# Kernel tuning notes

Hardware: AMD Instinct MI355X
Metric: run time of the kernel (lower is better)

Reference implementation:

```python
import jax, jax.numpy as jnp
import numpy as np

D_MODEL = 1024
NUM_HEADS = 16
HEAD_DIM = D_MODEL // NUM_HEADS
THETA = 10000.0
B, S = 1, 2048


def setup_inputs() -> dict:
    key = jax.random.key(0)
    ks = jax.random.split(key, 7)
    sc = 0.02
    return {
        "query": jax.random.normal(ks[0], (B, S, D_MODEL), jnp.float32),
        "key": jax.random.normal(ks[1], (B, S, D_MODEL), jnp.float32),
        "value": jax.random.normal(ks[2], (B, S, D_MODEL), jnp.float32),
        "qkv_w": jax.random.normal(ks[3], (3 * D_MODEL, D_MODEL), jnp.float32) * sc,
        "qkv_b": jax.random.normal(ks[4], (3 * D_MODEL,), jnp.float32) * sc,
        "out_w": jax.random.normal(ks[5], (D_MODEL, D_MODEL), jnp.float32) * sc,
        "out_b": jax.random.normal(ks[6], (D_MODEL,), jnp.float32) * sc,
    }


def _rope_cos_sin(seq_len, head_dim, dtype):
    # freqs_for='lang': inv_freq = theta^(-2i/d), i = 0..d/2-1
    inv_freq = 1.0 / (THETA ** (jnp.arange(0, head_dim, 2, dtype=jnp.float32) / head_dim))
    t = jnp.arange(seq_len, dtype=jnp.float32)
    freqs = jnp.outer(t, inv_freq)                      # [S, d/2]
    emb = jnp.concatenate([freqs, freqs], axis=-1)      # [S, d] (non-interleaved)
    return jnp.cos(emb).astype(dtype), jnp.sin(emb).astype(dtype)


def _rotate_half(x):
    half = x.shape[-1] // 2
    return jnp.concatenate([-x[..., half:], x[..., :half]], axis=-1)


def reference(query, key, value, qkv_w, qkv_b, out_w, out_b):
    # NOTE: module computes q,k,v all from `query` (key/value args unused).
    b, s, d = query.shape
    qkv = query @ qkv_w.T + qkv_b                       # [B,S,3D]
    qkv = qkv.reshape(b, s, 3, NUM_HEADS, HEAD_DIM)
    qkv = jnp.transpose(qkv, (2, 0, 3, 1, 4))           # [3,B,H,S,hd]
    q, k, v = qkv[0], qkv[1], qkv[2]

    cos, sin = _rope_cos_sin(s, HEAD_DIM, query.dtype)  # [S,hd]
    q = q * cos + _rotate_half(q) * sin
    k = k * cos + _rotate_half(k) * sin

    scale = 1.0 / np.sqrt(HEAD_DIM)
    scores = jnp.einsum('bhqd,bhkd->bhqk', q, k) * scale
    attn = jax.nn.softmax(scores, axis=-1)
    ctx = jnp.einsum('bhqk,bhkd->bhqd', attn, v)        # [B,H,S,hd]
    ctx = jnp.transpose(ctx, (0, 2, 1, 3)).reshape(b, s, d)
    return ctx @ out_w.T + out_b
```

## Files before the change

kernel.cpp:

```cpp
#include <hip/hip_runtime.h>
#include <math.h>
#include <stdint.h>

#define SEQ 2048
#define DM  1024
#define NH  16
#define HD  64
#define TRI 3072
#define NSPLIT 4

typedef _Float16 half8 __attribute__((ext_vector_type(8)));
typedef _Float16 half4 __attribute__((ext_vector_type(4)));
typedef __fp16 fp16x2 __attribute__((ext_vector_type(2)));
typedef float f32x4 __attribute__((ext_vector_type(4)));

#define GLOAD_LDS16(g, l)                                       \
  __builtin_amdgcn_global_load_lds(                             \
      (__attribute__((address_space(1))) void*)(g),             \
      (__attribute__((address_space(3))) void*)(l), 16, 0, 0)

#define QSCALE 0.18033688011112042f

__global__ __launch_bounds__(256)
void cvt3(const float* __restrict__ s1, const float* __restrict__ s2,
          const float* __restrict__ s3, _Float16* __restrict__ d1,
          _Float16* __restrict__ d2, _Float16* __restrict__ d3,
          float2* __restrict__ tab, int n1, int n2) {
  int b = blockIdx.x;
  if (b >= 6144) {
    int i = (b - 6144) * 256 + threadIdx.x;
    int s = i >> 5, d = i & 31;
    float inv = exp2f((float)d * -0.4152410118609203f);
    float ang = (float)s * inv;
    float sn, cs;
    sincosf(ang, &sn, &cs);
    tab[i] = make_float2(cs, sn);
    return;
  }
  int i = (b * 256 + threadIdx.x) * 4;
  const float* s; _Float16* d;
  if (i < n1)            { s = s1; d = d1; }
  else if (i < n1 + n2)  { s = s2; d = d2; i -= n1; }
  else                   { s = s3; d = d3; i -= n1 + n2; }
  float4 v = *(const float4*)(s + i);
  union { _Float16 h[4]; uint2 u; } pk;
  pk.h[0] = (_Float16)v.x; pk.h[1] = (_Float16)v.y;
  pk.h[2] = (_Float16)v.z; pk.h[3] = (_Float16)v.w;
  *(uint2*)(d + i) = pk.u;
}

__global__ __launch_bounds__(256)
void gemm_qkv(const _Float16* __restrict__ A, const _Float16* __restrict__ B,
              const float* __restrict__ bias, const float2* __restrict__ tab,
              _Float16* __restrict__ Qo, _Float16* __restrict__ Ko,
              _Float16* __restrict__ Vo) {
  constexpr int K = DM;
  __shared__ _Float16 As[2][64 * 32];
  __shared__ _Float16 Bs[2][128 * 32];

  const int t = threadIdx.x, lane = t & 63, wv = t >> 6;
  const int l15 = lane & 15, l4 = lane >> 4;
  const int wr = wv >> 1, wc = wv & 1;
  const int bm = blockIdx.y * 64, bn = blockIdx.x * 128;

  auto stage = [&](int buf, int k0) {
    {
      int c = t;
      GLOAD_LDS16(A + (size_t)(bm + (c >> 2)) * K + k0 + (c & 3) * 8,
                  (char*)&As[buf][wv * 512]);
    }
    #pragma unroll
    for (int i = 0; i < 2; ++i) {
      int c = t + i * 256;
      GLOAD_LDS16(B + (size_t)(bn + (c >> 2)) * K + k0 + (c & 3) * 8,
                  (char*)&Bs[buf][(i * 256 + wv * 64) * 8]);
    }
  };

  f32x4 acc[2][4] = {};
  stage(0, 0);
  __syncthreads();

  const int nk = K / 32;
  for (int s = 0; s < nk; ++s) {
    int cur = s & 1;
    if (s + 1 < nk) stage(cur ^ 1, (s + 1) * 32);
    half8 af[2], bf[4];
    #pragma unroll
    for (int mf = 0; mf < 2; ++mf)
      af[mf] = *(const half8*)&As[cur][(wr * 32 + mf * 16 + l15) * 32 + l4 * 8];
    #pragma unroll
    for (int nf = 0; nf < 4; ++nf)
      bf[nf] = *(const half8*)&Bs[cur][(wc * 64 + nf * 16 + l15) * 32 + l4 * 8];
    __builtin_amdgcn_s_setprio(1);
    #pragma unroll
    for (int mf = 0; mf < 2; ++mf)
      #pragma unroll
      for (int nf = 0; nf < 4; ++nf)
        acc[mf][nf] = __builtin_amdgcn_mfma_f32_16x16x32_f16(
            af[mf], bf[nf], acc[mf][nf], 0, 0, 0);
    __builtin_amdgcn_s_setprio(0);
    __syncthreads();
  }

  const int sec = bn >> 10;
  float bv[4];
  #pragma unroll
  for (int nf = 0; nf < 4; ++nf) bv[nf] = bias[bn + wc * 64 + nf * 16 + l15];

  if (sec == 0) {
    #pragma unroll
    for (int mf = 0; mf < 2; ++mf)
      #pragma unroll
      for (int r = 0; r < 4; ++r) {
        int row = bm + wr * 32 + mf * 16 + l4 * 4 + r;
        float v0 = acc[mf][0][r] + bv[0];
        float v1 = acc[mf][1][r] + bv[1];
        float v2 = acc[mf][2][r] + bv[2];
        float v3 = acc[mf][3][r] + bv[3];
        float2 cs0 = tab[row * 32 + l15];
        float2 cs1 = tab[row * 32 + 16 + l15];
        float a0 = (v0 * cs0.x - v2 * cs0.y) * QSCALE;
        float a2 = (v2 * cs0.x + v0 * cs0.y) * QSCALE;
        float a1 = (v1 * cs1.x - v3 * cs1.y) * QSCALE;
        float a3 = (v3 * cs1.x + v1 * cs1.y) * QSCALE;
        _Float16* cr = Qo + (size_t)row * DM + bn + wc * 64 + l15;
        cr[0]  = (_Float16)a0; cr[16] = (_Float16)a1;
        cr[32] = (_Float16)a2; cr[48] = (_Float16)a3;
      }
  } else if (sec == 1) {
    const int hh = ((bn - 1024) >> 6) + wc;
    const int e = l15 & 7, hi = l15 >> 3;
    #pragma unroll
    for (int mf = 0; mf < 2; ++mf)
      #pragma unroll
      for (int r = 0; r < 4; ++r) {
        int row = bm + wr * 32 + mf * 16 + l4 * 4 + r;
        float v0 = acc[mf][0][r] + bv[0];
        float v1 = acc[mf][1][r] + bv[1];
        float v2 = acc[mf][2][r] + bv[2];
        float v3 = acc[mf][3][r] + bv[3];
        float2 cs0 = tab[row * 32 + l15];
        float2 cs1 = tab[row * 32 + 16 + l15];
        float a0 = v0 * cs0.x - v2 * cs0.y;
        float a2 = v2 * cs0.x + v0 * cs0.y;
        float a1 = v1 * cs1.x - v3 * cs1.y;
        float a3 = v3 * cs1.x + v1 * cs1.y;
        int kk = row & 63, kseg = row >> 6;
        int hkk = (kk & 3) | ((kk >> 1) & 4);
        size_t base = ((size_t)(hh * 32 + kseg) * 64 + kk) * 64;
        Ko[base + (((0 + hi) ^ hkk) * 8) + e] = (_Float16)a0;
        Ko[base + (((2 + hi) ^ hkk) * 8) + e] = (_Float16)a1;
        Ko[base + (((4 + hi) ^ hkk) * 8) + e] = (_Float16)a2;
        Ko[base + (((6 + hi) ^ hkk) * 8) + e] = (_Float16)a3;
      }
  } else {
    const int hh = ((bn - 2048) >> 6) + wc;
    #pragma unroll
    for (int mf = 0; mf < 2; ++mf) {
      int row0 = bm + wr * 32 + mf * 16 + l4 * 4;
      int kk0 = row0 & 63, kseg = row0 >> 6;
      #pragma unroll
      for (int nf = 0; nf < 4; ++nf) {
        int d = nf * 16 + l15;
        union { _Float16 hh4[4]; uint2 u; } pk;
        #pragma unroll
        for (int r = 0; r < 4; ++r)
          pk.hh4[r] = (_Float16)(acc[mf][nf][r] + bv[nf]);
        size_t off = ((size_t)(hh * 32 + kseg) * 64 + d) * 64 +
                     (((kk0 >> 3) ^ (d & 7)) * 8) + (kk0 & 7);
        *(uint2*)(Vo + off) = pk.u;
      }
    }
  }
}

__global__ __launch_bounds__(256)
void gemm_out(const _Float16* __restrict__ A, const _Float16* __restrict__ B,
              const float* __restrict__ bias, float* __restrict__ C) {
  constexpr int K = DM, N = DM;
  __shared__ _Float16 As[2][64 * 32];
  __shared__ _Float16 Bs[2][128 * 32];

  const int t = threadIdx.x, lane = t & 63, wv = t >> 6;
  const int l15 = lane & 15, l4 = lane >> 4;
  const int wr = wv >> 1, wc = wv & 1;
  const int bm = blockIdx.y * 64, bn = blockIdx.x * 128;

  auto stage = [&](int buf, int k0) {
    {
      int c = t;
      GLOAD_LDS16(A + (size_t)(bm + (c >> 2)) * K + k0 + (c & 3) * 8,
                  (char*)&As[buf][wv * 512]);
    }
    #pragma unroll
    for (int i = 0; i < 2; ++i) {
      int c = t + i * 256;
      GLOAD_LDS16(B + (size_t)(bn + (c >> 2)) * K + k0 + (c & 3) * 8,
                  (char*)&Bs[buf][(i * 256 + wv * 64) * 8]);
    }
  };

  f32x4 acc[2][4] = {};
  stage(0, 0);
  __syncthreads();

  const int nk = K / 32;
  for (int s = 0; s < nk; ++s) {
    int cur = s & 1;
    if (s + 1 < nk) stage(cur ^ 1, (s + 1) * 32);
    half8 af[2], bf[4];
    #pragma unroll
    for (int mf = 0; mf < 2; ++mf)
      af[mf] = *(const half8*)&As[cur][(wr * 32 + mf * 16 + l15) * 32 + l4 * 8];
    #pragma unroll
    for (int nf = 0; nf < 4; ++nf)
      bf[nf] = *(const half8*)&Bs[cur][(wc * 64 + nf * 16 + l15) * 32 + l4 * 8];
    __builtin_amdgcn_s_setprio(1);
    #pragma unroll
    for (int mf = 0; mf < 2; ++mf)
      #pragma unroll
      for (int nf = 0; nf < 4; ++nf)
        acc[mf][nf] = __builtin_amdgcn_mfma_f32_16x16x32_f16(
            af[mf], bf[nf], acc[mf][nf], 0, 0, 0);
    __builtin_amdgcn_s_setprio(0);
    __syncthreads();
  }

  float bv[4];
  #pragma unroll
  for (int nf = 0; nf < 4; ++nf) bv[nf] = bias[bn + wc * 64 + nf * 16 + l15];
  #pragma unroll
  for (int mf = 0; mf < 2; ++mf)
    #pragma unroll
    for (int r = 0; r < 4; ++r) {
      int row = bm + wr * 32 + mf * 16 + l4 * 4 + r;
      float* cr = C + (size_t)row * N + bn + wc * 64 + l15;
      cr[0]  = acc[mf][0][r] + bv[0];
      cr[16] = acc[mf][1][r] + bv[1];
      cr[32] = acc[mf][2][r] + bv[2];
      cr[48] = acc[mf][3][r] + bv[3];
    }
}

__global__ __launch_bounds__(256)
void attn_f16(const _Float16* __restrict__ Qg, const _Float16* __restrict__ Kg,
              const _Float16* __restrict__ Vg, _Float16* __restrict__ poA,
              _Float16* __restrict__ po3, float* __restrict__ pl) {
  __shared__ _Float16 Kl[2][64 * 64];
  __shared__ _Float16 Vt[2][64 * 64];

  const int t = threadIdx.x, lane = t & 63, wv = t >> 6;
  const int l15 = lane & 15, l4 = lane >> 4;
  const int bid = blockIdx.x;
  const int c = bid & 63, qb = bid >> 6;
  const int h = c & 15, z = c >> 4;
  const int q0 = qb * 64;
  const int seg0 = z * (SEQ / NSPLIT / 64);

  const _Float16* Qp = Qg + h * HD;
  const _Float16* Kbase = Kg + (size_t)h * 32 * 4096;
  const _Float16* Vbase = Vg + (size_t)h * 32 * 4096;

  half8 qf[2];
  {
    const _Float16* qrow = Qp + (size_t)(q0 + wv * 16 + l15) * DM;
    qf[0] = *(const half8*)(qrow + l4 * 8);
    qf[1] = *(const half8*)(qrow + 32 + l4 * 8);
  }

  auto issueKV = [&](int buf, int seg) {
    const _Float16* ks = Kbase + (size_t)seg * 4096;
    const _Float16* vs = Vbase + (size_t)seg * 4096;
    GLOAD_LDS16(ks + (size_t)t * 8,         (char*)&Kl[buf][(wv * 64) * 8]);
    GLOAD_LDS16(ks + (size_t)(t + 256) * 8, (char*)&Kl[buf][(256 + wv * 64) * 8]);
    GLOAD_LDS16(vs + (size_t)t * 8,         (char*)&Vt[buf][(wv * 64) * 8]);
    GLOAD_LDS16(vs + (size_t)(t + 256) * 8, (char*)&Vt[buf][(256 + wv * 64) * 8]);
  };

  f32x4 lacc = {0.f, 0.f, 0.f, 0.f};
  f32x4 o[4] = {};

  const int hk = (l15 & 3) | (((l15 >> 2) & 1) << 2);
  const int krow = 8 * (l15 >> 2) + (l15 & 3);

  issueKV(0, seg0);

  const int NT = SEQ / NSPLIT / 64;
  #pragma unroll 2
  for (int tt = 0; tt < NT; ++tt) {
    const int cur = tt & 1;
    asm volatile("s_waitcnt vmcnt(0)" ::: "memory");
    __builtin_amdgcn_s_barrier();
    __builtin_amdgcn_sched_barrier(0);
    if (tt + 1 < NT) issueKV(cur ^ 1, seg0 + tt + 1);

    f32x4 sT[4] = {};
    __builtin_amdgcn_s_setprio(1);
    #pragma unroll
    for (int ds = 0; ds < 2; ++ds)
      #pragma unroll
      for (int m = 0; m < 4; ++m) {
        int kappa = 32 * (m >> 1) + 4 * (m & 1) + krow;
        int cb = ds * 4 + l4;
        half8 kf = *(const half8*)((char*)Kl[cur] + kappa * 128 +
                                   ((cb ^ hk) * 16));
        sT[m] = __builtin_amdgcn_mfma_f32_16x16x32_f16(kf, qf[ds], sT[m], 0, 0, 0);
      }
    __builtin_amdgcn_s_setprio(0);

    half8 pB[2];
    #pragma unroll
    for (int s2 = 0; s2 < 2; ++s2) {
      union { fp16x2 h2[4]; half8 v; } pu;
      #pragma unroll
      for (int mh = 0; mh < 2; ++mh) {
        int m = s2 * 2 + mh;
        f32x4 p;
        #pragma unroll
        for (int r = 0; r < 4; ++r) p[r] = exp2f(sT[m][r]);
        lacc += p;
        pu.h2[mh * 2 + 0] = __builtin_amdgcn_cvt_pkrtz(p[0], p[1]);
        pu.h2[mh * 2 + 1] = __builtin_amdgcn_cvt_pkrtz(p[2], p[3]);
      }
      pB[s2] = pu.v;
    }

    __builtin_amdgcn_s_setprio(1);
    #pragma unroll
    for (int s2 = 0; s2 < 2; ++s2)
      #pragma unroll
      for (int nf = 0; nf < 4; ++nf) {
        half8 va = *(const half8*)((char*)Vt[cur] + (nf * 16 + l15) * 128 +
                                   (((s2 * 4 + l4) ^ (l15 & 7)) * 16));
        o[nf] = __builtin_amdgcn_mfma_f32_16x16x32_f16(va, pB[s2], o[nf], 0, 0, 0);
      }
    __builtin_amdgcn_s_setprio(0);
  }

  float lv = (lacc[0] + lacc[1]) + (lacc[2] + lacc[3]);
  lv += __shfl_xor(lv, 16);
  lv += __shfl_xor(lv, 32);
  _Float16* pz = (z < 3) ? (poA + (size_t)z * SEQ * DM) : po3;
  {
    int row = q0 + wv * 16 + l15;
    _Float16* pr = pz + (size_t)row * DM + h * HD + l4 * 4;
    #pragma unroll
    for (int nf = 0; nf < 4; ++nf) {
      union { fp16x2 h2[2]; uint2 u; } ou;
      ou.h2[0] = __builtin_amdgcn_cvt_pkrtz(o[nf][0], o[nf][1]);
      ou.h2[1] = __builtin_amdgcn_cvt_pkrtz(o[nf][2], o[nf][3]);
      *(uint2*)(pr + nf * 16) = ou.u;
    }
  }
  if (l4 == 0) {
    int q = q0 + wv * 16 + l15;
    pl[(z * NH + h) * SEQ + q] = lv;
  }
}

__global__ __launch_bounds__(256)
void merge4(const _Float16* __restrict__ poA, const _Float16* __restrict__ po3,
            const float* __restrict__ pl, _Float16* __restrict__ ctx) {
  int e = (blockIdx.x * 256 + threadIdx.x) * 8;
  int s = e >> 10, h = (e & 1023) >> 6;
  int idx = h * SEQ + s;
  float L = pl[idx] + pl[NH * SEQ + idx] + pl[2 * NH * SEQ + idx] +
            pl[3 * NH * SEQ + idx];
  float inv = 1.0f / L;
  half8 a = *(const half8*)(poA + e);
  half8 b = *(const half8*)(poA + (size_t)SEQ * DM + e);
  half8 cc = *(const half8*)(poA + 2 * (size_t)SEQ * DM + e);
  half8 d = *(const half8*)(po3 + e);
  half8 o;
  #pragma unroll
  for (int j = 0; j < 8; ++j)
    o[j] = (_Float16)((((float)a[j] + (float)b[j]) +
                       ((float)cc[j] + (float)d[j])) * inv);
  *(half8*)(ctx + e) = o;
}

extern "C" void kernel_launch(void* const* d_in, const int* in_sizes, int n_in,
                              void* d_out, int out_size, void* d_ws, size_t ws_size,
                              hipStream_t stream) {
  const float* query = (const float*)d_in[0];
  const float* qkv_w = (const float*)d_in[3];
  const float* qkv_b = (const float*)d_in[4];
  const float* out_w = (const float*)d_in[5];
  const float* out_b = (const float*)d_in[6];
  float* out = (float*)d_out;

  char* ws = (char*)d_ws;
  _Float16* Aq   = (_Float16*)ws;
  _Float16* Wqkv = (_Float16*)(ws + (4u << 20));
  _Float16* Qb   = (_Float16*)(ws + (12u << 20));
  _Float16* Kb   = (_Float16*)(ws + (16u << 20));
  _Float16* Vb   = (_Float16*)(ws + (20u << 20));
  _Float16* ctx  = (_Float16*)(ws + (24u << 20));
  float2*   tab  = (float2*)(ws + (28u << 20));
  _Float16* Wout = (_Float16*)(ws + (28u << 20) + (512u << 10));
  float*    pl   = (float*)(ws + (30u << 20) + (512u << 10));
  _Float16* poA  = (_Float16*)ws;
  _Float16* po3  = ctx;

  cvt3<<<6400, 256, 0, stream>>>(query, qkv_w, out_w, Aq, Wqkv, Wout, tab,
                                 SEQ * DM, TRI * DM);

  gemm_qkv<<<dim3(TRI / 128, SEQ / 64), 256, 0, stream>>>(
      Aq, Wqkv, qkv_b, tab, Qb, Kb, Vb);

  attn_f16<<<(SEQ / 64) * NH * NSPLIT, 256, 0, stream>>>(
      Qb, Kb, Vb, poA, po3, pl);

  merge4<<<SEQ * DM / 8 / 256, 256, 0, stream>>>(poA, po3, pl, ctx);

  gemm_out<<<dim3(DM / 128, SEQ / 64), 256, 0, stream>>>(ctx, Wout, out_b, out);
}
```

Before: 96.90 us.

## Fuse split-merge into output GEMM, enlarge QKV tiles, widen attention blocks

```diff
diff --git a/kernel.cpp b/kernel.cpp
--- a/kernel.cpp
+++ b/kernel.cpp
@@ -10,7 +10,6 @@
 #define NSPLIT 4
 
 typedef _Float16 half8 __attribute__((ext_vector_type(8)));
-typedef _Float16 half4 __attribute__((ext_vector_type(4)));
 typedef __fp16 fp16x2 __attribute__((ext_vector_type(2)));
 typedef float f32x4 __attribute__((ext_vector_type(4)));
 
@@ -55,19 +54,20 @@
               _Float16* __restrict__ Qo, _Float16* __restrict__ Ko,
               _Float16* __restrict__ Vo) {
   constexpr int K = DM;
-  __shared__ _Float16 As[2][64 * 32];
-  __shared__ _Float16 Bs[2][128 * 32];
+  __shared__ _Float16 As[3][128 * 32];
+  __shared__ _Float16 Bs[3][128 * 32];
 
   const int t = threadIdx.x, lane = t & 63, wv = t >> 6;
   const int l15 = lane & 15, l4 = lane >> 4;
   const int wr = wv >> 1, wc = wv & 1;
-  const int bm = blockIdx.y * 64, bn = blockIdx.x * 128;
+  const int bm = blockIdx.y * 128, bn = blockIdx.x * 128;
 
   auto stage = [&](int buf, int k0) {
-    {
-      int c = t;
+    #pragma unroll
+    for (int i = 0; i < 2; ++i) {
+      int c = t + i * 256;
       GLOAD_LDS16(A + (size_t)(bm + (c >> 2)) * K + k0 + (c & 3) * 8,
-                  (char*)&As[buf][wv * 512]);
+                  (char*)&As[buf][(i * 256 + wv * 64) * 8]);
     }
     #pragma unroll
     for (int i = 0; i < 2; ++i) {
@@ -77,30 +77,34 @@
     }
   };
 
-  f32x4 acc[2][4] = {};
+  f32x4 acc[4][4] = {};
   stage(0, 0);
-  __syncthreads();
+  stage(1, 32);
 
   const int nk = K / 32;
   for (int s = 0; s < nk; ++s) {
-    int cur = s & 1;
-    if (s + 1 < nk) stage(cur ^ 1, (s + 1) * 32);
-    half8 af[2], bf[4];
-    #pragma unroll
-    for (int mf = 0; mf < 2; ++mf)
-      af[mf] = *(const half8*)&As[cur][(wr * 32 + mf * 16 + l15) * 32 + l4 * 8];
+    int cur = s % 3;
+    if (s + 1 < nk) asm volatile("s_waitcnt vmcnt(4)" ::: "memory");
+    else            asm volatile("s_waitcnt vmcnt(0)" ::: "memory");
+    __builtin_amdgcn_s_barrier();
+    __builtin_amdgcn_sched_barrier(0);
+    if (s + 2 < nk) stage((s + 2) % 3, (s + 2) * 32);
+
+    half8 af[4], bf[4];
+    #pragma unroll
+    for (int mf = 0; mf < 4; ++mf)
+      af[mf] = *(const half8*)&As[cur][(wr * 64 + mf * 16 + l15) * 32 + l4 * 8];
     #pragma unroll
     for (int nf = 0; nf < 4; ++nf)
       bf[nf] = *(const half8*)&Bs[cur][(wc * 64 + nf * 16 + l15) * 32 + l4 * 8];
     __builtin_amdgcn_s_setprio(1);
     #pragma unroll
-    for (int mf = 0; mf < 2; ++mf)
+    for (int mf = 0; mf < 4; ++mf)
       #pragma unroll
       for (int nf = 0; nf < 4; ++nf)
         acc[mf][nf] = __builtin_amdgcn_mfma_f32_16x16x32_f16(
             af[mf], bf[nf], acc[mf][nf], 0, 0, 0);
     __builtin_amdgcn_s_setprio(0);
-    __syncthreads();
   }
 
   const int sec = bn >> 10;
@@ -108,34 +112,13 @@
   #pragma unroll
   for (int nf = 0; nf < 4; ++nf) bv[nf] = bias[bn + wc * 64 + nf * 16 + l15];
 
-  if (sec == 0) {
-    #pragma unroll
-    for (int mf = 0; mf < 2; ++mf)
+  if (sec < 2) {
+    _Float16* dst = (sec == 0) ? Qo : Ko;
+    #pragma unroll
+    for (int mf = 0; mf < 4; ++mf)
       #pragma unroll
       for (int r = 0; r < 4; ++r) {
-        int row = bm + wr * 32 + mf * 16 + l4 * 4 + r;
-        float v0 = acc[mf][0][r] + bv[0];
-        float v1 = acc[mf][1][r] + bv[1];
-        float v2 = acc[mf][2][r] + bv[2];
-        float v3 = acc[mf][3][r] + bv[3];
-        float2 cs0 = tab[row * 32 + l15];
-        float2 cs1 = tab[row * 32 + 16 + l15];
-        float a0 = (v0 * cs0.x - v2 * cs0.y) * QSCALE;
-        float a2 = (v2 * cs0.x + v0 * cs0.y) * QSCALE;
-        float a1 = (v1 * cs1.x - v3 * cs1.y) * QSCALE;
-        float a3 = (v3 * cs1.x + v1 * cs1.y) * QSCALE;
-        _Float16* cr = Qo + (size_t)row * DM + bn + wc * 64 + l15;
-        cr[0]  = (_Float16)a0; cr[16] = (_Float16)a1;
-        cr[32] = (_Float16)a2; cr[48] = (_Float16)a3;
-      }
-  } else if (sec == 1) {
-    const int hh = ((bn - 1024) >> 6) + wc;
-    const int e = l15 & 7, hi = l15 >> 3;
-    #pragma unroll
-    for (int mf = 0; mf < 2; ++mf)
-      #pragma unroll
-      for (int r = 0; r < 4; ++r) {
-        int row = bm + wr * 32 + mf * 16 + l4 * 4 + r;
+        int row = bm + wr * 64 + mf * 16 + l4 * 4 + r;
         float v0 = acc[mf][0][r] + bv[0];
         float v1 = acc[mf][1][r] + bv[1];
         float v2 = acc[mf][2][r] + bv[2];
@@ -146,19 +129,16 @@
         float a2 = v2 * cs0.x + v0 * cs0.y;
         float a1 = v1 * cs1.x - v3 * cs1.y;
         float a3 = v3 * cs1.x + v1 * cs1.y;
-        int kk = row & 63, kseg = row >> 6;
-        int hkk = (kk & 3) | ((kk >> 1) & 4);
-        size_t base = ((size_t)(hh * 32 + kseg) * 64 + kk) * 64;
-        Ko[base + (((0 + hi) ^ hkk) * 8) + e] = (_Float16)a0;
-        Ko[base + (((2 + hi) ^ hkk) * 8) + e] = (_Float16)a1;
-        Ko[base + (((4 + hi) ^ hkk) * 8) + e] = (_Float16)a2;
-        Ko[base + (((6 + hi) ^ hkk) * 8) + e] = (_Float16)a3;
+        if (sec == 0) { a0 *= QSCALE; a1 *= QSCALE; a2 *= QSCALE; a3 *= QSCALE; }
+        _Float16* cr = dst + (size_t)row * DM + (bn & 1023) + wc * 64 + l15;
+        cr[0]  = (_Float16)a0; cr[16] = (_Float16)a1;
+        cr[32] = (_Float16)a2; cr[48] = (_Float16)a3;
       }
   } else {
     const int hh = ((bn - 2048) >> 6) + wc;
     #pragma unroll
-    for (int mf = 0; mf < 2; ++mf) {
-      int row0 = bm + wr * 32 + mf * 16 + l4 * 4;
+    for (int mf = 0; mf < 4; ++mf) {
+      int row0 = bm + wr * 64 + mf * 16 + l4 * 4;
       int kk0 = row0 & 63, kseg = row0 >> 6;
       #pragma unroll
       for (int nf = 0; nf < 4; ++nf) {
@@ -175,75 +155,7 @@
   }
 }
 
-__global__ __launch_bounds__(256)
-void gemm_out(const _Float16* __restrict__ A, const _Float16* __restrict__ B,
-              const float* __restrict__ bias, float* __restrict__ C) {
-  constexpr int K = DM, N = DM;
-  __shared__ _Float16 As[2][64 * 32];
-  __shared__ _Float16 Bs[2][128 * 32];
-
-  const int t = threadIdx.x, lane = t & 63, wv = t >> 6;
-  const int l15 = lane & 15, l4 = lane >> 4;
-  const int wr = wv >> 1, wc = wv & 1;
-  const int bm = blockIdx.y * 64, bn = blockIdx.x * 128;
-
-  auto stage = [&](int buf, int k0) {
-    {
-      int c = t;
-      GLOAD_LDS16(A + (size_t)(bm + (c >> 2)) * K + k0 + (c & 3) * 8,
-                  (char*)&As[buf][wv * 512]);
-    }
-    #pragma unroll
-    for (int i = 0; i < 2; ++i) {
-      int c = t + i * 256;
-      GLOAD_LDS16(B + (size_t)(bn + (c >> 2)) * K + k0 + (c & 3) * 8,
-                  (char*)&Bs[buf][(i * 256 + wv * 64) * 8]);
-    }
-  };
-
-  f32x4 acc[2][4] = {};
-  stage(0, 0);
-  __syncthreads();
-
-  const int nk = K / 32;
-  for (int s = 0; s < nk; ++s) {
-    int cur = s & 1;
-    if (s + 1 < nk) stage(cur ^ 1, (s + 1) * 32);
-    half8 af[2], bf[4];
-    #pragma unroll
-    for (int mf = 0; mf < 2; ++mf)
-      af[mf] = *(const half8*)&As[cur][(wr * 32 + mf * 16 + l15) * 32 + l4 * 8];
-    #pragma unroll
-    for (int nf = 0; nf < 4; ++nf)
-      bf[nf] = *(const half8*)&Bs[cur][(wc * 64 + nf * 16 + l15) * 32 + l4 * 8];
-    __builtin_amdgcn_s_setprio(1);
-    #pragma unroll
-    for (int mf = 0; mf < 2; ++mf)
-      #pragma unroll
-      for (int nf = 0; nf < 4; ++nf)
-        acc[mf][nf] = __builtin_amdgcn_mfma_f32_16x16x32_f16(
-            af[mf], bf[nf], acc[mf][nf], 0, 0, 0);
-    __builtin_amdgcn_s_setprio(0);
-    __syncthreads();
-  }
-
-  float bv[4];
-  #pragma unroll
-  for (int nf = 0; nf < 4; ++nf) bv[nf] = bias[bn + wc * 64 + nf * 16 + l15];
-  #pragma unroll
-  for (int mf = 0; mf < 2; ++mf)
-    #pragma unroll
-    for (int r = 0; r < 4; ++r) {
-      int row = bm + wr * 32 + mf * 16 + l4 * 4 + r;
-      float* cr = C + (size_t)row * N + bn + wc * 64 + l15;
-      cr[0]  = acc[mf][0][r] + bv[0];
-      cr[16] = acc[mf][1][r] + bv[1];
-      cr[32] = acc[mf][2][r] + bv[2];
-      cr[48] = acc[mf][3][r] + bv[3];
-    }
-}
-
-__global__ __launch_bounds__(256)
+__global__ __launch_bounds__(512)
 void attn_f16(const _Float16* __restrict__ Qg, const _Float16* __restrict__ Kg,
               const _Float16* __restrict__ Vg, _Float16* __restrict__ poA,
               _Float16* __restrict__ po3, float* __restrict__ pl) {
@@ -255,11 +167,11 @@
   const int bid = blockIdx.x;
   const int c = bid & 63, qb = bid >> 6;
   const int h = c & 15, z = c >> 4;
-  const int q0 = qb * 64;
+  const int q0 = qb * 128;
   const int seg0 = z * (SEQ / NSPLIT / 64);
 
   const _Float16* Qp = Qg + h * HD;
-  const _Float16* Kbase = Kg + (size_t)h * 32 * 4096;
+  const _Float16* Kp = Kg + h * HD;
   const _Float16* Vbase = Vg + (size_t)h * 32 * 4096;
 
   half8 qf[2];
@@ -269,13 +181,18 @@
     qf[1] = *(const half8*)(qrow + 32 + l4 * 8);
   }
 
+  int koff;
+  {
+    int kk = t >> 3, p = t & 7;
+    int hkk = (kk & 3) | ((kk >> 1) & 4);
+    koff = kk * DM + ((p ^ hkk) * 8);
+  }
+
   auto issueKV = [&](int buf, int seg) {
-    const _Float16* ks = Kbase + (size_t)seg * 4096;
+    const _Float16* ks = Kp + (size_t)seg * 64 * DM;
     const _Float16* vs = Vbase + (size_t)seg * 4096;
-    GLOAD_LDS16(ks + (size_t)t * 8,         (char*)&Kl[buf][(wv * 64) * 8]);
-    GLOAD_LDS16(ks + (size_t)(t + 256) * 8, (char*)&Kl[buf][(256 + wv * 64) * 8]);
-    GLOAD_LDS16(vs + (size_t)t * 8,         (char*)&Vt[buf][(wv * 64) * 8]);
-    GLOAD_LDS16(vs + (size_t)(t + 256) * 8, (char*)&Vt[buf][(256 + wv * 64) * 8]);
+    GLOAD_LDS16(ks + koff,          (char*)&Kl[buf][(wv * 64) * 8]);
+    GLOAD_LDS16(vs + (size_t)t * 8, (char*)&Vt[buf][(wv * 64) * 8]);
   };
 
   f32x4 lacc = {0.f, 0.f, 0.f, 0.f};
@@ -360,24 +277,111 @@
 }
 
 __global__ __launch_bounds__(256)
-void merge4(const _Float16* __restrict__ poA, const _Float16* __restrict__ po3,
-            const float* __restrict__ pl, _Float16* __restrict__ ctx) {
-  int e = (blockIdx.x * 256 + threadIdx.x) * 8;
-  int s = e >> 10, h = (e & 1023) >> 6;
-  int idx = h * SEQ + s;
-  float L = pl[idx] + pl[NH * SEQ + idx] + pl[2 * NH * SEQ + idx] +
-            pl[3 * NH * SEQ + idx];
-  float inv = 1.0f / L;
-  half8 a = *(const half8*)(poA + e);
-  half8 b = *(const half8*)(poA + (size_t)SEQ * DM + e);
-  half8 cc = *(const half8*)(poA + 2 * (size_t)SEQ * DM + e);
-  half8 d = *(const half8*)(po3 + e);
-  half8 o;
+void gemm_out_merge(const _Float16* __restrict__ poA,
+                    const _Float16* __restrict__ po3,
+                    const float* __restrict__ pl,
+                    const _Float16* __restrict__ Bw,
+                    const float* __restrict__ bias,
+                    float* __restrict__ C) {
+  constexpr int K = DM, N = DM;
+  __shared__ _Float16 As[2][64 * 32];
+  __shared__ _Float16 Bs[2][128 * 32];
+  __shared__ float Ls[64 * 16];
+
+  const int t = threadIdx.x, lane = t & 63, wv = t >> 6;
+  const int l15 = lane & 15, l4 = lane >> 4;
+  const int wr = wv >> 1, wc = wv & 1;
+  const int bm = blockIdx.y * 64, bn = blockIdx.x * 128;
+
+  auto stageB = [&](int buf, int k0) {
+    #pragma unroll
+    for (int i = 0; i < 2; ++i) {
+      int c = t + i * 256;
+      GLOAD_LDS16(Bw + (size_t)(bn + (c >> 2)) * K + k0 + (c & 3) * 8,
+                  (char*)&Bs[buf][(i * 256 + wv * 64) * 8]);
+    }
+  };
+
+  const int arow = t >> 2;
+  const size_t abase = (size_t)(bm + arow) * DM + (t & 3) * 8;
+
+  half8 a0, a1, a2, a3;
+  auto loadA = [&](int k0) {
+    const _Float16* p = poA + abase + k0;
+    a0 = *(const half8*)p;
+    a1 = *(const half8*)(p + (size_t)SEQ * DM);
+    a2 = *(const half8*)(p + 2 * (size_t)SEQ * DM);
+    a3 = *(const half8*)(po3 + abase + k0);
+  };
+  auto writeA = [&](int buf, int k0) {
+    float inv = Ls[arow * 16 + (k0 >> 6)];
+    union { fp16x2 h2[4]; half8 v; } m;
+    #pragma unroll
+    for (int j = 0; j < 4; ++j) {
+      float lo = ((float)a0[2 * j] + (float)a1[2 * j] +
+                  (float)a2[2 * j] + (float)a3[2 * j]) * inv;
+      float hi = ((float)a0[2 * j + 1] + (float)a1[2 * j + 1] +
+                  (float)a2[2 * j + 1] + (float)a3[2 * j + 1]) * inv;
+      m.h2[j] = __builtin_amdgcn_cvt_pkrtz(lo, hi);
+    }
+    *(half8*)((char*)As[buf] + t * 16) = m.v;
+  };
+
+  stageB(0, 0);
   #pragma unroll
-  for (int j = 0; j < 8; ++j)
-    o[j] = (_Float16)((((float)a[j] + (float)b[j]) +
-                       ((float)cc[j] + (float)d[j])) * inv);
-  *(half8*)(ctx + e) = o;
+  for (int i = 0; i < 4; ++i) {
+    int e = t + i * 256;
+    int row = e >> 4, hh = e & 15;
+    int s = bm + row;
+    float L = pl[hh * SEQ + s] + pl[(NH + hh) * SEQ + s] +
+              pl[(2 * NH + hh) * SEQ + s] + pl[(3 * NH + hh) * SEQ + s];
+    Ls[e] = 1.0f / L;
+  }
+  loadA(0);
+  __syncthreads();
+  writeA(0, 0);
+  __syncthreads();
+
+  f32x4 acc[2][4] = {};
+  const int nk = K / 32;
+  for (int s = 0; s < nk; ++s) {
+    int cur = s & 1;
+    if (s + 1 < nk) { stageB(cur ^ 1, (s + 1) * 32); loadA((s + 1) * 32); }
+
+    half8 af[2], bf[4];
+    #pragma unroll
+    for (int mf = 0; mf < 2; ++mf)
+      af[mf] = *(const half8*)&As[cur][(wr * 32 + mf * 16 + l15) * 32 + l4 * 8];
+    #pragma unroll
+    for (int nf = 0; nf < 4; ++nf)
+      bf[nf] = *(const half8*)&Bs[cur][(wc * 64 + nf * 16 + l15) * 32 + l4 * 8];
+    __builtin_amdgcn_s_setprio(1);
+    #pragma unroll
+    for (int mf = 0; mf < 2; ++mf)
+      #pragma unroll
+      for (int nf = 0; nf < 4; ++nf)
+        acc[mf][nf] = __builtin_amdgcn_mfma_f32_16x16x32_f16(
+            af[mf], bf[nf], acc[mf][nf], 0, 0, 0);
+    __builtin_amdgcn_s_setprio(0);
+
+    if (s + 1 < nk) writeA(cur ^ 1, (s + 1) * 32);
+    __syncthreads();
+  }
+
+  float bv[4];
+  #pragma unroll
+  for (int nf = 0; nf < 4; ++nf) bv[nf] = bias[bn + wc * 64 + nf * 16 + l15];
+  #pragma unroll
+  for (int mf = 0; mf < 2; ++mf)
+    #pragma unroll
+    for (int r = 0; r < 4; ++r) {
+      int row = bm + wr * 32 + mf * 16 + l4 * 4 + r;
+      float* cr = C + (size_t)row * N + bn + wc * 64 + l15;
+      cr[0]  = acc[mf][0][r] + bv[0];
+      cr[16] = acc[mf][1][r] + bv[1];
+      cr[32] = acc[mf][2][r] + bv[2];
+      cr[48] = acc[mf][3][r] + bv[3];
+    }
 }
 
 extern "C" void kernel_launch(void* const* d_in, const int* in_sizes, int n_in,
@@ -396,23 +400,21 @@
   _Float16* Qb   = (_Float16*)(ws + (12u << 20));
   _Float16* Kb   = (_Float16*)(ws + (16u << 20));
   _Float16* Vb   = (_Float16*)(ws + (20u << 20));
-  _Float16* ctx  = (_Float16*)(ws + (24u << 20));
+  _Float16* po3  = (_Float16*)(ws + (24u << 20));
   float2*   tab  = (float2*)(ws + (28u << 20));
   _Float16* Wout = (_Float16*)(ws + (28u << 20) + (512u << 10));
   float*    pl   = (float*)(ws + (30u << 20) + (512u << 10));
   _Float16* poA  = (_Float16*)ws;
-  _Float16* po3  = ctx;
 
   cvt3<<<6400, 256, 0, stream>>>(query, qkv_w, out_w, Aq, Wqkv, Wout, tab,
                                  SEQ * DM, TRI * DM);
 
-  gemm_qkv<<<dim3(TRI / 128, SEQ / 64), 256, 0, stream>>>(
+  gemm_qkv<<<dim3(TRI / 128, SEQ / 128), 256, 0, stream>>>(
       Aq, Wqkv, qkv_b, tab, Qb, Kb, Vb);
 
-  attn_f16<<<(SEQ / 64) * NH * NSPLIT, 256, 0, stream>>>(
+  attn_f16<<<(SEQ / 128) * NH * NSPLIT, 512, 0, stream>>>(
       Qb, Kb, Vb, poA, po3, pl);
 
-  merge4<<<SEQ * DM / 8 / 256, 256, 0, stream>>>(poA, po3, pl, ctx);
-
-  gemm_out<<<dim3(DM / 128, SEQ / 64), 256, 0, stream>>>(ctx, Wout, out_b, out);
+  gemm_out_merge<<<dim3(DM / 128, SEQ / 64), 256, 0, stream>>>(
+      poA, po3, pl, Wout, out_b, out);
 }
```

Result: slower. 104.9 us (+8.3%).
